# Kernel tuning notes

Measured on AMD Instinct MI355X. Metric: run time of the kernel, lower is better.

The kernel has to match this reference:

```python
import jax, jax.numpy as jnp
import numpy as np

EPS = 1e-5

def _act_quant(x):
    # per-token int8 absmax quantization with STE passthrough
    s = 127.0 / jnp.clip(jnp.max(jnp.abs(x), axis=-1, keepdims=True), EPS, None)
    xq = jnp.clip(jnp.round(x * s), -128.0, 127.0) / s
    return x + jax.lax.stop_gradient(xq - x)

def _weight_quant(w):
    # ternary {-1,0,1} abs-mean quantization with STE passthrough
    s = 1.0 / jnp.clip(jnp.mean(jnp.abs(w)), EPS, None)
    wq = jnp.clip(jnp.round(w * s), -1.0, 1.0) / s
    return w + jax.lax.stop_gradient(wq - w)

def bitlinear(x, w, b=None):
    y = _act_quant(x) @ _weight_quant(w).T
    return y if b is None else y + b

def setup_inputs() -> dict:
    key = jax.random.key(0)
    ks = jax.random.split(key, 6)
    B, T, C = 64, 256, 1024
    std = 1.0 / np.sqrt(C)
    return {
        "x": jax.random.normal(ks[0], (B, T, C), dtype=jnp.float32),
        "Wq": jax.random.normal(ks[1], (C, C), dtype=jnp.float32) * std,
        "Wk": jax.random.normal(ks[2], (C, C), dtype=jnp.float32) * std,
        "Wv": jax.random.normal(ks[3], (C, C), dtype=jnp.float32) * std,
        "Wp": jax.random.normal(ks[4], (C, C), dtype=jnp.float32) * std,
        "bp": jnp.zeros((C,), dtype=jnp.float32),
        "n_head": 16,
    }

def reference(x, Wq, Wk, Wv, Wp, bp, n_head):
    B, T, C = x.shape
    hd = C // n_head
    def heads(t):  # [B,T,C] -> [B,H,T,hd]
        return t.reshape(B, T, n_head, hd).transpose(0, 2, 1, 3)
    q = heads(bitlinear(x, Wq))
    k = heads(bitlinear(x, Wk))
    v = heads(bitlinear(x, Wv))
    attn = jnp.einsum("bhqd,bhkd->bhqk", q, k) * (1.0 / np.sqrt(hd))
    causal = jnp.tril(jnp.ones((T, T), dtype=bool))
    attn = jnp.where(causal, attn, -jnp.inf)
    attn = jax.nn.softmax(attn, axis=-1)
    y = jnp.einsum("bhqk,bhkd->bhqd", attn, v)
    y = y.transpose(0, 2, 1, 3).reshape(B, T, C)
    return bitlinear(y, Wp, bp)
```

## Files before the change

### kernel.cpp

```cpp
#include <hip/hip_runtime.h>
#include <math.h>

#define AS1 __attribute__((address_space(1)))
#define AS3 __attribute__((address_space(3)))

typedef unsigned short u16;
typedef signed char i8;
typedef short bf16x8 __attribute__((ext_vector_type(8)));
typedef float f32x4 __attribute__((ext_vector_type(4)));
typedef int i32x4 __attribute__((ext_vector_type(4)));

static constexpr int BB = 64, T = 256, C = 1024, H = 16, HD = 64;
static constexpr int M = BB * T;
static constexpr float EPSF = 1e-5f;

static constexpr size_t W8_OFF   = 0;
static constexpr size_t XQ8_OFF  = 4ull  << 20;
static constexpr size_t RSX_OFF  = 20ull << 20;
static constexpr size_t RSY_OFF  = (20ull << 20) + (64 << 10);
static constexpr size_t WSUM_OFF = (20ull << 20) + (128 << 10);
static constexpr size_t WPART_OFF= WSUM_OFF + 64;
static constexpr size_t QB_OFF   = 21ull << 20;
static constexpr size_t KB_OFF   = 53ull << 20;
static constexpr size_t VT_OFF   = 85ull << 20;

__device__ __forceinline__ u16 f2bf_rne(float f) {
    unsigned x = __float_as_uint(f);
    unsigned r = x + 0x7FFF + ((x >> 16) & 1);
    return (u16)(r >> 16);
}

__global__ __launch_bounds__(256) void wsum1_kernel(const float* __restrict__ Wq,
    const float* __restrict__ Wk, const float* __restrict__ Wv,
    const float* __restrict__ Wp, double* __restrict__ wpart)
{
    const int mat = blockIdx.x >> 6;
    const float* W = (mat == 0) ? Wq : (mat == 1) ? Wk : (mat == 2) ? Wv : Wp;
    const int t = threadIdx.x;
    const int base = (blockIdx.x & 63) * 256 + t;
    double s = 0.0;
    for (int i = 0; i < 64; ++i) s += (double)fabsf(W[base + (i << 14)]);
    #pragma unroll
    for (int off = 32; off >= 1; off >>= 1) s += __shfl_down(s, off);
    __shared__ double red[4];
    if ((t & 63) == 0) red[t >> 6] = s;
    __syncthreads();
    if (t == 0) wpart[blockIdx.x] = red[0] + red[1] + red[2] + red[3];
}

__global__ __launch_bounds__(256) void wsum2_kernel(const double* __restrict__ wpart,
                                                    double* __restrict__ wsum)
{
    const int t = threadIdx.x;
    double s = wpart[t];
    #pragma unroll
    for (int off = 32; off >= 1; off >>= 1) s += __shfl_down(s, off);
    if ((t & 63) == 0) wsum[t >> 6] = s;
}

__global__ __launch_bounds__(256) void wquant_kernel(const float* __restrict__ Wq,
    const float* __restrict__ Wk, const float* __restrict__ Wv,
    const float* __restrict__ Wp, const double* __restrict__ wsum,
    i8* __restrict__ w8)
{
    const int mat = blockIdx.x >> 10;
    const float* W = (mat == 0) ? Wq : (mat == 1) ? Wk : (mat == 2) ? Wv : Wp;
    const float mean = (float)(wsum[mat] * (1.0 / 1048576.0));
    const float s = 1.0f / fmaxf(mean, EPSF);
    const int idx = (blockIdx.x & 1023) * 256 + threadIdx.x;
    float4 w = ((const float4*)W)[idx];
    char4 o;
    o.x = (i8)(int)fminf(fmaxf(rintf(w.x * s), -1.f), 1.f);
    o.y = (i8)(int)fminf(fmaxf(rintf(w.y * s), -1.f), 1.f);
    o.z = (i8)(int)fminf(fmaxf(rintf(w.z * s), -1.f), 1.f);
    o.w = (i8)(int)fminf(fmaxf(rintf(w.w * s), -1.f), 1.f);
    ((char4*)(w8 + (size_t)mat * 1048576))[idx] = o;
}

__global__ __launch_bounds__(256) void actquant_kernel(const float* __restrict__ x,
    i8* __restrict__ xq, float* __restrict__ rs)
{
    const int row = blockIdx.x;
    const int t = threadIdx.x;
    float4 v = ((const float4*)(x + (size_t)row * C))[t];
    float m = fmaxf(fmaxf(fabsf(v.x), fabsf(v.y)), fmaxf(fabsf(v.z), fabsf(v.w)));
    #pragma unroll
    for (int off = 32; off >= 1; off >>= 1) m = fmaxf(m, __shfl_down(m, off));
    __shared__ float red[4];
    if ((t & 63) == 0) red[t >> 6] = m;
    __syncthreads();
    float mm = fmaxf(fmaxf(red[0], red[1]), fmaxf(red[2], red[3]));
    mm = fmaxf(mm, EPSF);
    const float s = 127.0f / mm;
    if (t == 0) rs[row] = mm / 127.0f;
    char4 o;
    o.x = (i8)(int)fminf(fmaxf(rintf(v.x * s), -128.f), 127.f);
    o.y = (i8)(int)fminf(fmaxf(rintf(v.y * s), -128.f), 127.f);
    o.z = (i8)(int)fminf(fmaxf(rintf(v.z * s), -128.f), 127.f);
    o.w = (i8)(int)fminf(fmaxf(rintf(v.w * s), -128.f), 127.f);
    ((char4*)(xq + (size_t)row * C))[t] = o;
}

template<bool QKV>
__global__ __launch_bounds__(256) void gemm_kernel(const i8* __restrict__ A,
    const i8* __restrict__ w8, const float* __restrict__ rs_row,
    const double* __restrict__ wsum, u16* __restrict__ qb, u16* __restrict__ kb,
    u16* __restrict__ vt, float* __restrict__ outp, const float* __restrict__ bias)
{
    constexpr int K = 1024, N = 1024;
    __shared__ __align__(16) i8 Asm[128 * 64];
    __shared__ __align__(16) i8 Bsm[128 * 64];

    const int t = threadIdx.x;
    const int m0 = blockIdx.y * 128;
    const int nb  = QKV ? (int)(blockIdx.x & 7) : (int)blockIdx.x;
    const int mat = QKV ? (int)(blockIdx.x >> 3) : 3;
    const int n0 = nb * 128;
    const i8* Bw = w8 + (size_t)mat * 1048576;

    const int lane = t & 63, wave = t >> 6;
    const int wm = wave >> 1, wn = wave & 1;
    const int mr = lane & 15, quad = lane >> 4;

    i32x4 acc[4][4];
    #pragma unroll
    for (int i = 0; i < 4; ++i)
        #pragma unroll
        for (int j = 0; j < 4; ++j) acc[i][j] = (i32x4){0, 0, 0, 0};

    const int c0 = t, c1 = t + 256;
    const int r0 = c0 >> 2, g0 = ((c0 & 3) ^ ((r0 >> 1) & 3)) * 16;
    const int r1 = c1 >> 2, g1 = ((c1 & 3) ^ ((r1 >> 1) & 3)) * 16;
    const i8* a0 = A  + (size_t)(m0 + r0) * K + g0;
    const i8* a1 = A  + (size_t)(m0 + r1) * K + g1;
    const i8* b0 = Bw + (size_t)(n0 + r0) * K + g0;
    const i8* b1 = Bw + (size_t)(n0 + r1) * K + g1;

    const int swq = (quad ^ ((mr >> 1) & 3)) * 16;

    for (int k0 = 0; k0 < K; k0 += 64) {
        __builtin_amdgcn_global_load_lds((const AS1 void*)(a0 + k0), (AS3 void*)&Asm[c0 * 16], 16, 0, 0);
        __builtin_amdgcn_global_load_lds((const AS1 void*)(a1 + k0), (AS3 void*)&Asm[c1 * 16], 16, 0, 0);
        __builtin_amdgcn_global_load_lds((const AS1 void*)(b0 + k0), (AS3 void*)&Bsm[c0 * 16], 16, 0, 0);
        __builtin_amdgcn_global_load_lds((const AS1 void*)(b1 + k0), (AS3 void*)&Bsm[c1 * 16], 16, 0, 0);
        __syncthreads();
        i32x4 af[4], bf[4];
        #pragma unroll
        for (int i = 0; i < 4; ++i)
            af[i] = *(const i32x4*)&Asm[(wm * 64 + i * 16 + mr) * 64 + swq];
        #pragma unroll
        for (int j = 0; j < 4; ++j)
            bf[j] = *(const i32x4*)&Bsm[(wn * 64 + j * 16 + mr) * 64 + swq];
        #pragma unroll
        for (int i = 0; i < 4; ++i)
            #pragma unroll
            for (int j = 0; j < 4; ++j)
                acc[i][j] = __builtin_amdgcn_mfma_i32_16x16x64_i8(af[i], bf[j], acc[i][j], 0, 0, 0);
        __syncthreads();
    }

    float wsc = fmaxf((float)(wsum[mat] * (1.0 / 1048576.0)), EPSF);
    if (QKV && mat == 0) wsc *= 0.125f;

    if (QKV && mat == 2) {
        #pragma unroll
        for (int i = 0; i < 4; ++i) {
            const int gr0 = m0 + wm * 64 + i * 16 + quad * 4;
            const int bb = gr0 >> 8, tl = gr0 & 255;
            const float4 rs4 = *(const float4*)(rs_row + gr0);
            #pragma unroll
            for (int j = 0; j < 4; ++j) {
                const int gcol = n0 + wn * 64 + j * 16 + mr;
                ushort4 o;
                o.x = f2bf_rne((float)acc[i][j][0] * rs4.x * wsc);
                o.y = f2bf_rne((float)acc[i][j][1] * rs4.y * wsc);
                o.z = f2bf_rne((float)acc[i][j][2] * rs4.z * wsc);
                o.w = f2bf_rne((float)acc[i][j][3] * rs4.w * wsc);
                *(ushort4*)(vt + (size_t)(bb * 1024 + gcol) * 256 + tl) = o;
            }
        }
        return;
    }

    u16* ob = QKV ? ((mat == 0) ? qb : kb) : nullptr;
    #pragma unroll
    for (int i = 0; i < 4; ++i) {
        const int gr0 = m0 + wm * 64 + i * 16 + quad * 4;
        #pragma unroll
        for (int r = 0; r < 4; ++r) {
            const int grow = gr0 + r;
            const float sc = rs_row[grow] * wsc;
            #pragma unroll
            for (int j = 0; j < 4; ++j) {
                const int gcol = n0 + wn * 64 + j * 16 + mr;
                const float vv = (float)acc[i][j][r] * sc;
                if (QKV) {
                    ob[(size_t)grow * N + gcol] = f2bf_rne(vv);
                } else {
                    outp[(size_t)grow * N + gcol] = vv + bias[gcol];
                }
            }
        }
    }
}

__global__ __launch_bounds__(256) void attn_kernel(const u16* __restrict__ qb,
    const u16* __restrict__ kb, const u16* __restrict__ vt, float* __restrict__ y)
{
    const int t = threadIdx.x;
    const int qt = 3 - (int)(blockIdx.x >> 10);
    const int bh = blockIdx.x & 1023;
    const int b = bh >> 4, h = bh & 15;
    const int w = t >> 6, lane = t & 63;
    const int cl = lane & 15, quad = lane >> 4;
    const size_t gb = (size_t)(b * T) * 1024 + h * 64;
    const u16* vtb = vt + (size_t)(b * 1024 + h * 64) * 256;

    const int qrow = qt * 64 + w * 16;
    const int jtiles = (qrow >> 4) + 1;

    const u16* qrp = qb + gb + (size_t)(qrow + cl) * 1024 + quad * 8;
    bf16x8 qf0 = *(const bf16x8*)qrp;
    bf16x8 qf1 = *(const bf16x8*)(qrp + 32);

    f32x4 Sp[16];
    #pragma unroll
    for (int i = 0; i < 16; ++i) Sp[i] = (f32x4){0.f, 0.f, 0.f, 0.f};

    const u16* krp = kb + gb + (size_t)cl * 1024 + quad * 8;
    #pragma unroll
    for (int jt = 0; jt < 16; ++jt) {
        if (jt < jtiles) {
            const u16* kp = krp + (size_t)(jt * 16) * 1024;
            bf16x8 kf0 = *(const bf16x8*)kp;
            bf16x8 kf1 = *(const bf16x8*)(kp + 32);
            Sp[jt] = __builtin_amdgcn_mfma_f32_16x16x32_bf16(kf0, qf0, Sp[jt], 0, 0, 0);
            Sp[jt] = __builtin_amdgcn_mfma_f32_16x16x32_bf16(kf1, qf1, Sp[jt], 0, 0, 0);
            if (jt == jtiles - 1) {
                #pragma unroll
                for (int r = 0; r < 4; ++r)
                    if (quad * 4 + r > cl) Sp[jt][r] = -INFINITY;
            }
        }
    }

    float mx = -INFINITY;
    #pragma unroll
    for (int jt = 0; jt < 16; ++jt) if (jt < jtiles) {
        #pragma unroll
        for (int r = 0; r < 4; ++r) mx = fmaxf(mx, Sp[jt][r]);
    }
    mx = fmaxf(mx, __shfl_xor(mx, 16));
    mx = fmaxf(mx, __shfl_xor(mx, 32));
    float l = 0.f;
    #pragma unroll
    for (int jt = 0; jt < 16; ++jt) if (jt < jtiles) {
        #pragma unroll
        for (int r = 0; r < 4; ++r) {
            float p = __expf(Sp[jt][r] - mx);
            Sp[jt][r] = p;
            l += p;
        }
    }
    l += __shfl_xor(l, 16);
    l += __shfl_xor(l, 32);

    f32x4 O[4];
    #pragma unroll
    for (int i = 0; i < 4; ++i) O[i] = (f32x4){0.f, 0.f, 0.f, 0.f};

    const int s01 = ((quad & 1) << 5) + cl;
    const bool lo = quad < 2;
    #pragma unroll
    for (int jc = 0; jc < 8; ++jc) {
        if (jc * 2 < jtiles) {
            int pk[2][2];
            #pragma unroll
            for (int s = 0; s < 2; ++s) {
                const f32x4 v = Sp[jc * 2 + s];
                pk[s][0] = (int)((unsigned)f2bf_rne(v[0]) | ((unsigned)f2bf_rne(v[1]) << 16));
                pk[s][1] = (int)((unsigned)f2bf_rne(v[2]) | ((unsigned)f2bf_rne(v[3]) << 16));
            }
            int a0 = __shfl(pk[0][0], s01),      a1 = __shfl(pk[0][1], s01);
            int a2 = __shfl(pk[0][0], s01 + 16), a3 = __shfl(pk[0][1], s01 + 16);
            int b0 = __shfl(pk[1][0], s01),      b1 = __shfl(pk[1][1], s01);
            int b2 = __shfl(pk[1][0], s01 + 16), b3 = __shfl(pk[1][1], s01 + 16);
            union { int i[4]; bf16x8 v; } af;
            af.i[0] = lo ? a0 : b0;
            af.i[1] = lo ? a1 : b1;
            af.i[2] = lo ? a2 : b2;
            af.i[3] = lo ? a3 : b3;
            const u16* vp = vtb + (size_t)cl * 256 + jc * 32 + quad * 8;
            #pragma unroll
            for (int dt = 0; dt < 4; ++dt) {
                bf16x8 vf = *(const bf16x8*)(vp + (size_t)dt * 16 * 256);
                O[dt] = __builtin_amdgcn_mfma_f32_16x16x32_bf16(af.v, vf, O[dt], 0, 0, 0);
            }
        }
    }

    float inv[4];
    #pragma unroll
    for (int r = 0; r < 4; ++r) inv[r] = 1.0f / __shfl(l, quad * 4 + r);
    #pragma unroll
    for (int dt = 0; dt < 4; ++dt)
        #pragma unroll
        for (int r = 0; r < 4; ++r)
            y[gb + (size_t)(qrow + quad * 4 + r) * 1024 + dt * 16 + cl] = O[dt][r] * inv[r];
}

extern "C" void kernel_launch(void* const* d_in, const int* in_sizes, int n_in,
                              void* d_out, int out_size, void* d_ws, size_t ws_size,
                              hipStream_t stream) {
    (void)in_sizes; (void)n_in; (void)out_size; (void)ws_size;
    const float* x  = (const float*)d_in[0];
    const float* Wq = (const float*)d_in[1];
    const float* Wk = (const float*)d_in[2];
    const float* Wv = (const float*)d_in[3];
    const float* Wp = (const float*)d_in[4];
    const float* bp = (const float*)d_in[5];
    float* out = (float*)d_out;
    char* ws = (char*)d_ws;

    i8*     w8   = (i8*)(ws + W8_OFF);
    i8*     xq8  = (i8*)(ws + XQ8_OFF);
    float*  rsx  = (float*)(ws + RSX_OFF);
    float*  rsy  = (float*)(ws + RSY_OFF);
    double* wsum = (double*)(ws + WSUM_OFF);
    double* wpart= (double*)(ws + WPART_OFF);
    u16*    qb   = (u16*)(ws + QB_OFF);
    u16*    kb   = (u16*)(ws + KB_OFF);
    u16*    vt   = (u16*)(ws + VT_OFF);

    wsum1_kernel<<<256, 256, 0, stream>>>(Wq, Wk, Wv, Wp, wpart);
    wsum2_kernel<<<1, 256, 0, stream>>>(wpart, wsum);
    wquant_kernel<<<4096, 256, 0, stream>>>(Wq, Wk, Wv, Wp, wsum, w8);
    actquant_kernel<<<M, 256, 0, stream>>>(x, xq8, rsx);

    gemm_kernel<true ><<<dim3(24, 128), 256, 0, stream>>>(xq8, w8, rsx, wsum, qb, kb, vt, nullptr, nullptr);

    attn_kernel<<<4 * 1024, 256, 0, stream>>>(qb, kb, vt, out);

    actquant_kernel<<<M, 256, 0, stream>>>(out, xq8, rsy);
    gemm_kernel<false><<<dim3(8, 128), 256, 0, stream>>>(xq8, w8, rsy, wsum, nullptr, nullptr, nullptr, out, bp);
}
```

Before: 337.2 us.

## Rewrite int8 GEMM with 256x256 tiles, 4-stage LDS pipeline and XCD swizzle

```diff
diff --git a/kernel.cpp b/kernel.cpp
--- a/kernel.cpp
+++ b/kernel.cpp
@@ -101,62 +101,115 @@
     ((char4*)(xq + (size_t)row * C))[t] = o;
 }
 
-template<bool QKV>
-__global__ __launch_bounds__(256) void gemm_kernel(const i8* __restrict__ A,
+template<bool QKV, int NNB>
+__global__ __launch_bounds__(512, 2) void gemm_kernel(const i8* __restrict__ A,
     const i8* __restrict__ w8, const float* __restrict__ rs_row,
     const double* __restrict__ wsum, u16* __restrict__ qb, u16* __restrict__ kb,
     u16* __restrict__ vt, float* __restrict__ outp, const float* __restrict__ bias)
 {
     constexpr int K = 1024, N = 1024;
-    __shared__ __align__(16) i8 Asm[128 * 64];
-    __shared__ __align__(16) i8 Bsm[128 * 64];
-
-    const int t = threadIdx.x;
-    const int m0 = blockIdx.y * 128;
-    const int nb  = QKV ? (int)(blockIdx.x & 7) : (int)blockIdx.x;
-    const int mat = QKV ? (int)(blockIdx.x >> 3) : 3;
-    const int n0 = nb * 128;
+    constexpr int NT = 16;
+    __shared__ __align__(16) i8 Asm[4][256 * 64];
+    __shared__ __align__(16) i8 Bsm[4][256 * 64];
+
+    const int t = threadIdx.x;
+
+    const int nwg = NNB * 64;
+    const int wg = (int)blockIdx.x;
+    const int swz = (wg & 7) * (nwg >> 3) + (wg >> 3);
+    const int mb = swz / NNB, nb = swz % NNB;
+    const int m0 = mb * 256;
+    const int mat = QKV ? (nb >> 2) : 3;
+    const int n0m = QKV ? ((nb & 3) * 256) : (nb * 256);
     const i8* Bw = w8 + (size_t)mat * 1048576;
 
-    const int lane = t & 63, wave = t >> 6;
-    const int wm = wave >> 1, wn = wave & 1;
+    const int lane = t & 63, wv = t >> 6;
+    const int wm = wv >> 2, wn = wv & 3;
     const int mr = lane & 15, quad = lane >> 4;
 
-    i32x4 acc[4][4];
-    #pragma unroll
-    for (int i = 0; i < 4; ++i)
-        #pragma unroll
-        for (int j = 0; j < 4; ++j) acc[i][j] = (i32x4){0, 0, 0, 0};
-
-    const int c0 = t, c1 = t + 256;
-    const int r0 = c0 >> 2, g0 = ((c0 & 3) ^ ((r0 >> 1) & 3)) * 16;
-    const int r1 = c1 >> 2, g1 = ((c1 & 3) ^ ((r1 >> 1) & 3)) * 16;
-    const i8* a0 = A  + (size_t)(m0 + r0) * K + g0;
-    const i8* a1 = A  + (size_t)(m0 + r1) * K + g1;
-    const i8* b0 = Bw + (size_t)(n0 + r0) * K + g0;
-    const i8* b1 = Bw + (size_t)(n0 + r1) * K + g1;
-
-    const int swq = (quad ^ ((mr >> 1) & 3)) * 16;
-
-    for (int k0 = 0; k0 < K; k0 += 64) {
-        __builtin_amdgcn_global_load_lds((const AS1 void*)(a0 + k0), (AS3 void*)&Asm[c0 * 16], 16, 0, 0);
-        __builtin_amdgcn_global_load_lds((const AS1 void*)(a1 + k0), (AS3 void*)&Asm[c1 * 16], 16, 0, 0);
-        __builtin_amdgcn_global_load_lds((const AS1 void*)(b0 + k0), (AS3 void*)&Bsm[c0 * 16], 16, 0, 0);
-        __builtin_amdgcn_global_load_lds((const AS1 void*)(b1 + k0), (AS3 void*)&Bsm[c1 * 16], 16, 0, 0);
-        __syncthreads();
-        i32x4 af[4], bf[4];
-        #pragma unroll
-        for (int i = 0; i < 4; ++i)
-            af[i] = *(const i32x4*)&Asm[(wm * 64 + i * 16 + mr) * 64 + swq];
-        #pragma unroll
-        for (int j = 0; j < 4; ++j)
-            bf[j] = *(const i32x4*)&Bsm[(wn * 64 + j * 16 + mr) * 64 + swq];
-        #pragma unroll
-        for (int i = 0; i < 4; ++i)
-            #pragma unroll
-            for (int j = 0; j < 4; ++j)
-                acc[i][j] = __builtin_amdgcn_mfma_i32_16x16x64_i8(af[i], bf[j], acc[i][j], 0, 0, 0);
-        __syncthreads();
+    const int g1 = t, g2 = t + 512;
+    const int L1 = (g1 * 16) ^ (((g1 >> 3) & 7) << 4);
+    const int L2 = (g2 * 16) ^ (((g2 >> 3) & 7) << 4);
+    const i8* a1 = A  + (size_t)(m0  + (L1 >> 6)) * K + (L1 & 63);
+    const i8* a2 = A  + (size_t)(m0  + (L2 >> 6)) * K + (L2 & 63);
+    const i8* b1 = Bw + (size_t)(n0m + (L1 >> 6)) * K + (L1 & 63);
+    const i8* b2 = Bw + (size_t)(n0m + (L2 >> 6)) * K + (L2 & 63);
+
+    const int vvs = (mr >> 1) & 7;
+    int aoff[8], boff[4];
+    #pragma unroll
+    for (int m = 0; m < 8; ++m)
+        aoff[m] = ((wm * 128 + m * 16 + mr) * 64 + quad * 16) ^ (vvs << 4);
+    #pragma unroll
+    for (int n = 0; n < 4; ++n)
+        boff[n] = ((wn * 64 + n * 16 + mr) * 64 + quad * 16) ^ (vvs << 4);
+
+    i32x4 acc[8][4];
+    #pragma unroll
+    for (int m = 0; m < 8; ++m)
+        #pragma unroll
+        for (int n = 0; n < 4; ++n) acc[m][n] = (i32x4){0, 0, 0, 0};
+
+    #pragma unroll
+    for (int p = 0; p < 2; ++p) {
+        const int k0 = p * 64;
+        __builtin_amdgcn_global_load_lds((const AS1 void*)(a1 + k0), (AS3 void*)&Asm[p][g1 * 16], 16, 0, 0);
+        __builtin_amdgcn_global_load_lds((const AS1 void*)(a2 + k0), (AS3 void*)&Asm[p][g2 * 16], 16, 0, 0);
+        __builtin_amdgcn_global_load_lds((const AS1 void*)(b1 + k0), (AS3 void*)&Bsm[p][g1 * 16], 16, 0, 0);
+        __builtin_amdgcn_global_load_lds((const AS1 void*)(b2 + k0), (AS3 void*)&Bsm[p][g2 * 16], 16, 0, 0);
+    }
+    asm volatile("s_waitcnt vmcnt(4)" ::: "memory");
+    __builtin_amdgcn_s_barrier();
+
+    for (int tt = 0; tt < NT; ++tt) {
+        const i8* Ac = Asm[tt & 3];
+        const i8* Bc = Bsm[tt & 3];
+        i8* An = Asm[(tt + 2) & 3];
+        i8* Bn = Bsm[(tt + 2) & 3];
+        const int kn = (tt + 2) * 64;
+        const bool pf = (tt < NT - 2);
+
+        if (pf) {
+            __builtin_amdgcn_global_load_lds((const AS1 void*)(a1 + kn), (AS3 void*)&An[g1 * 16], 16, 0, 0);
+            __builtin_amdgcn_global_load_lds((const AS1 void*)(a2 + kn), (AS3 void*)&An[g2 * 16], 16, 0, 0);
+        }
+        i32x4 af[8];
+        #pragma unroll
+        for (int m = 0; m < 8; ++m) af[m] = *(const i32x4*)&Ac[aoff[m]];
+        i32x4 bf0 = *(const i32x4*)&Bc[boff[0]];
+        i32x4 bf1 = *(const i32x4*)&Bc[boff[1]];
+        __builtin_amdgcn_s_barrier();
+        asm volatile("s_waitcnt lgkmcnt(0)" ::: "memory");
+        __builtin_amdgcn_s_setprio(1);
+        #pragma unroll
+        for (int m = 0; m < 8; ++m) {
+            acc[m][0] = __builtin_amdgcn_mfma_i32_16x16x64_i8(af[m], bf0, acc[m][0], 0, 0, 0);
+            acc[m][1] = __builtin_amdgcn_mfma_i32_16x16x64_i8(af[m], bf1, acc[m][1], 0, 0, 0);
+        }
+        __builtin_amdgcn_s_setprio(0);
+        __builtin_amdgcn_s_barrier();
+
+        if (pf) {
+            __builtin_amdgcn_global_load_lds((const AS1 void*)(b1 + kn), (AS3 void*)&Bn[g1 * 16], 16, 0, 0);
+            __builtin_amdgcn_global_load_lds((const AS1 void*)(b2 + kn), (AS3 void*)&Bn[g2 * 16], 16, 0, 0);
+        }
+        i32x4 bf2 = *(const i32x4*)&Bc[boff[2]];
+        i32x4 bf3 = *(const i32x4*)&Bc[boff[3]];
+        __builtin_amdgcn_s_barrier();
+        asm volatile("s_waitcnt lgkmcnt(0)" ::: "memory");
+        __builtin_amdgcn_s_setprio(1);
+        #pragma unroll
+        for (int m = 0; m < 8; ++m) {
+            acc[m][2] = __builtin_amdgcn_mfma_i32_16x16x64_i8(af[m], bf2, acc[m][2], 0, 0, 0);
+            acc[m][3] = __builtin_amdgcn_mfma_i32_16x16x64_i8(af[m], bf3, acc[m][3], 0, 0, 0);
+        }
+        __builtin_amdgcn_s_setprio(0);
+        if (tt < NT - 2) {
+            asm volatile("s_waitcnt vmcnt(4)" ::: "memory");
+        } else if (tt < NT - 1) {
+            asm volatile("s_waitcnt vmcnt(0)" ::: "memory");
+        }
+        __builtin_amdgcn_s_barrier();
     }
 
     float wsc = fmaxf((float)(wsum[mat] * (1.0 / 1048576.0)), EPSF);
@@ -164,19 +217,19 @@
 
     if (QKV && mat == 2) {
         #pragma unroll
-        for (int i = 0; i < 4; ++i) {
-            const int gr0 = m0 + wm * 64 + i * 16 + quad * 4;
-            const int bb = gr0 >> 8, tl = gr0 & 255;
+        for (int m = 0; m < 8; ++m) {
+            const int gr0 = m0 + wm * 128 + m * 16 + quad * 4;
+            const int bbi = gr0 >> 8, tl = gr0 & 255;
             const float4 rs4 = *(const float4*)(rs_row + gr0);
             #pragma unroll
-            for (int j = 0; j < 4; ++j) {
-                const int gcol = n0 + wn * 64 + j * 16 + mr;
+            for (int n = 0; n < 4; ++n) {
+                const int gcol = n0m + wn * 64 + n * 16 + mr;
                 ushort4 o;
-                o.x = f2bf_rne((float)acc[i][j][0] * rs4.x * wsc);
-                o.y = f2bf_rne((float)acc[i][j][1] * rs4.y * wsc);
-                o.z = f2bf_rne((float)acc[i][j][2] * rs4.z * wsc);
-                o.w = f2bf_rne((float)acc[i][j][3] * rs4.w * wsc);
-                *(ushort4*)(vt + (size_t)(bb * 1024 + gcol) * 256 + tl) = o;
+                o.x = f2bf_rne((float)acc[m][n][0] * rs4.x * wsc);
+                o.y = f2bf_rne((float)acc[m][n][1] * rs4.y * wsc);
+                o.z = f2bf_rne((float)acc[m][n][2] * rs4.z * wsc);
+                o.w = f2bf_rne((float)acc[m][n][3] * rs4.w * wsc);
+                *(ushort4*)(vt + (size_t)(bbi * 1024 + gcol) * 256 + tl) = o;
             }
         }
         return;
@@ -184,20 +237,20 @@
 
     u16* ob = QKV ? ((mat == 0) ? qb : kb) : nullptr;
     #pragma unroll
-    for (int i = 0; i < 4; ++i) {
-        const int gr0 = m0 + wm * 64 + i * 16 + quad * 4;
+    for (int m = 0; m < 8; ++m) {
+        const int gr0 = m0 + wm * 128 + m * 16 + quad * 4;
         #pragma unroll
         for (int r = 0; r < 4; ++r) {
             const int grow = gr0 + r;
             const float sc = rs_row[grow] * wsc;
             #pragma unroll
-            for (int j = 0; j < 4; ++j) {
-                const int gcol = n0 + wn * 64 + j * 16 + mr;
-                const float vv = (float)acc[i][j][r] * sc;
+            for (int n = 0; n < 4; ++n) {
+                const int gcol = n0m + wn * 64 + n * 16 + mr;
+                const float val = (float)acc[m][n][r] * sc;
                 if (QKV) {
-                    ob[(size_t)grow * N + gcol] = f2bf_rne(vv);
+                    ob[(size_t)grow * N + gcol] = f2bf_rne(val);
                 } else {
-                    outp[(size_t)grow * N + gcol] = vv + bias[gcol];
+                    outp[(size_t)grow * N + gcol] = val + bias[gcol];
                 }
             }
         }
@@ -337,10 +390,10 @@
     wquant_kernel<<<4096, 256, 0, stream>>>(Wq, Wk, Wv, Wp, wsum, w8);
     actquant_kernel<<<M, 256, 0, stream>>>(x, xq8, rsx);
 
-    gemm_kernel<true ><<<dim3(24, 128), 256, 0, stream>>>(xq8, w8, rsx, wsum, qb, kb, vt, nullptr, nullptr);
+    gemm_kernel<true, 12><<<768, 512, 0, stream>>>(xq8, w8, rsx, wsum, qb, kb, vt, nullptr, nullptr);
 
     attn_kernel<<<4 * 1024, 256, 0, stream>>>(qb, kb, vt, out);
 
     actquant_kernel<<<M, 256, 0, stream>>>(out, xq8, rsy);
-    gemm_kernel<false><<<dim3(8, 128), 256, 0, stream>>>(xq8, w8, rsy, wsum, nullptr, nullptr, nullptr, out, bp);
-}
+    gemm_kernel<false, 4><<<256, 512, 0, stream>>>(xq8, w8, rsy, wsum, nullptr, nullptr, nullptr, out, bp);
+}
```

After: 322.0 us. 1.05x faster.
